# Performance work log

Measured on AMD Instinct MI355X. Metric: run time of the kernel, lower is better.

The kernel has to match this reference:

```python
import jax, jax.numpy as jnp
import numpy as np

N_GENE, N_CELL, D, E = 20000, 50000, 256, 300000

def setup_inputs() -> dict:
    key = jax.random.key(0)
    k1, k2, k3, k4 = jax.random.split(key, 4)
    ufeat = jax.random.normal(k1, (N_GENE, D), dtype=jnp.float32)
    ifeat = jax.random.normal(k2, (N_CELL, D), dtype=jnp.float32)
    src = jax.random.randint(k3, (E,), 0, N_GENE, dtype=jnp.int64 if jax.config.jax_enable_x64 else jnp.int32)
    dst = jax.random.randint(k4, (E,), 0, N_CELL, dtype=jnp.int64 if jax.config.jax_enable_x64 else jnp.int32)
    return {"ufeat": ufeat, "ifeat": ifeat, "src": src, "dst": dst}

def reference(ufeat, ifeat, src, dst):
    # BiDecoder.forward actually executed path: dropout(rate=0.0) == identity,
    # then DGL fn.u_dot_v('h','h','sr') and immediate return of graph.edata['sr'].
    # Per-edge gather + dot product -> shape (E, 1)
    hu = jnp.take(ufeat, src, axis=0)  # (E, D)
    hv = jnp.take(ifeat, dst, axis=0)  # (E, D)
    return jnp.sum(hu * hv, axis=1, keepdims=True)  # (E, 1)
```

## Files before the change

kernel.cpp:

```cpp
#include <hip/hip_runtime.h>
#include <hip/hip_bf16.h>


typedef _Float16 half4 __attribute__((ext_vector_type(4)));
typedef _Float16 half8 __attribute__((ext_vector_type(8)));

__global__ __launch_bounds__(256) void cvt_f32_to_f16(
    const float* __restrict__ u, const float* __restrict__ v,
    _Float16* __restrict__ uh, _Float16* __restrict__ vh,
    int nU, int nTotal)
{
    int i = blockIdx.x * blockDim.x + threadIdx.x;
    const int stride = gridDim.x * blockDim.x;
    const int total8 = nTotal / 8;
    for (; i < total8; i += stride) {
        const int j = i * 8;
        const float* sp;
        _Float16* dp;
        if (j < nU) { sp = u + j;        dp = uh + j; }
        else        { sp = v + (j - nU); dp = vh + (j - nU); }
        const float4 f0 = *reinterpret_cast<const float4*>(sp);
        const float4 f1 = *reinterpret_cast<const float4*>(sp + 4);
        half8 h;
        h[0] = (_Float16)f0.x; h[1] = (_Float16)f0.y;
        h[2] = (_Float16)f0.z; h[3] = (_Float16)f0.w;
        h[4] = (_Float16)f1.x; h[5] = (_Float16)f1.y;
        h[6] = (_Float16)f1.z; h[7] = (_Float16)f1.w;
        *reinterpret_cast<half8*>(dp) = h;
    }
}

__global__ __launch_bounds__(256) void edge_dot_f16(
    const _Float16* __restrict__ uh,
    const _Float16* __restrict__ vh,
    const int* __restrict__ src,
    const int* __restrict__ dst,
    float* __restrict__ out,
    int E)
{
    const int wid  = (blockIdx.x * blockDim.x + threadIdx.x) >> 6;
    const int lane = threadIdx.x & 63;
    const int e0   = wid * 4;
    if (e0 >= E) return;

    const size_t lo = (size_t)lane * 4;

    if (e0 + 3 < E) {
        const int4 sv = *reinterpret_cast<const int4*>(src + e0);
        const int4 tv = *reinterpret_cast<const int4*>(dst + e0);

        const half4 a0 = *reinterpret_cast<const half4*>(uh + (size_t)sv.x * 256 + lo);
        const half4 b0 = *reinterpret_cast<const half4*>(vh + (size_t)tv.x * 256 + lo);
        const half4 a1 = *reinterpret_cast<const half4*>(uh + (size_t)sv.y * 256 + lo);
        const half4 b1 = *reinterpret_cast<const half4*>(vh + (size_t)tv.y * 256 + lo);
        const half4 a2 = *reinterpret_cast<const half4*>(uh + (size_t)sv.z * 256 + lo);
        const half4 b2 = *reinterpret_cast<const half4*>(vh + (size_t)tv.z * 256 + lo);
        const half4 a3 = *reinterpret_cast<const half4*>(uh + (size_t)sv.w * 256 + lo);
        const half4 b3 = *reinterpret_cast<const half4*>(vh + (size_t)tv.w * 256 + lo);

        float u0 = 0.f, u1 = 0.f, u2 = 0.f, u3 = 0.f;
        #pragma unroll
        for (int k = 0; k < 4; ++k) {
            u0 += (float)a0[k] * (float)b0[k];
            u1 += (float)a1[k] * (float)b1[k];
            u2 += (float)a2[k] * (float)b2[k];
            u3 += (float)a3[k] * (float)b3[k];
        }

        #pragma unroll
        for (int off = 32; off > 0; off >>= 1) {
            u0 += __shfl_xor(u0, off, 64);
            u1 += __shfl_xor(u1, off, 64);
            u2 += __shfl_xor(u2, off, 64);
            u3 += __shfl_xor(u3, off, 64);
        }

        float v = u0;
        v = (lane == 1) ? u1 : v;
        v = (lane == 2) ? u2 : v;
        v = (lane == 3) ? u3 : v;
        if (lane < 4) out[e0 + lane] = v;
    } else {
        for (int e = e0; e < E; ++e) {
            const half4 a = *reinterpret_cast<const half4*>(uh + (size_t)src[e] * 256 + lo);
            const half4 b = *reinterpret_cast<const half4*>(vh + (size_t)dst[e] * 256 + lo);
            float u = 0.f;
            #pragma unroll
            for (int k = 0; k < 4; ++k) u += (float)a[k] * (float)b[k];
            #pragma unroll
            for (int off = 32; off > 0; off >>= 1) u += __shfl_xor(u, off, 64);
            if (lane == 0) out[e] = u;
        }
    }
}

__global__ __launch_bounds__(256) void edge_dot_f32(
    const float* __restrict__ ufeat,
    const float* __restrict__ ifeat,
    const int* __restrict__ src,
    const int* __restrict__ dst,
    float* __restrict__ out,
    int E)
{
    const int wid  = (blockIdx.x * blockDim.x + threadIdx.x) >> 6;
    const int lane = threadIdx.x & 63;
    const int e0   = wid * 4;
    if (e0 >= E) return;
    const size_t lo = (size_t)lane * 4;

    for (int e = e0; e < min(e0 + 4, E); ++e) {
        const float4 a = *reinterpret_cast<const float4*>(ufeat + (size_t)src[e] * 256 + lo);
        const float4 b = *reinterpret_cast<const float4*>(ifeat + (size_t)dst[e] * 256 + lo);
        float u = a.x*b.x + a.y*b.y + a.z*b.z + a.w*b.w;
        #pragma unroll
        for (int off = 32; off > 0; off >>= 1) u += __shfl_xor(u, off, 64);
        if (lane == 0) out[e] = u;
    }
}

extern "C" void kernel_launch(void* const* d_in, const int* in_sizes, int n_in,
                              void* d_out, int out_size, void* d_ws, size_t ws_size,
                              hipStream_t stream)
{
    const float* ufeat = (const float*)d_in[0];
    const float* ifeat = (const float*)d_in[1];
    const int*   src   = (const int*)d_in[2];
    const int*   dst   = (const int*)d_in[3];
    float*       out   = (float*)d_out;

    const int E  = in_sizes[2];
    const int nU = in_sizes[0];
    const int nV = in_sizes[1];
    const size_t needBytes = (size_t)(nU + nV) * sizeof(_Float16);

    const int block = 256;
    const int edgesPerBlock = (block / 64) * 4;
    const int grid = (E + edgesPerBlock - 1) / edgesPerBlock;

    if (ws_size >= needBytes) {
        _Float16* uh = (_Float16*)d_ws;
        _Float16* vh = uh + nU;

        const int cvtGrid = 2048;
        cvt_f32_to_f16<<<cvtGrid, block, 0, stream>>>(ufeat, ifeat, uh, vh,
                                                      nU, nU + nV);
        edge_dot_f16<<<grid, block, 0, stream>>>(uh, vh, src, dst, out, E);
    } else {
        edge_dot_f32<<<grid, block, 0, stream>>>(ufeat, ifeat, src, dst, out, E);
    }
}
```

Measured before the change: 60.72 us.

## Bucket edges by destination row range across blocks for L2 locality

The edge-dot kernel now launches 8 blocks per 128-edge chunk. Each block handles only the edges whose destination row falls in its eighth of the cell table, which is meant to make the vh gathers hit a smaller L2/MALL-resident working set. The f32-to-f16 conversion also switches to nontemporal loads. The cost is that every block reads the full dst index array (8x index traffic) and computes per-edge divisions and branches. Each wave also processes edges one at a time with a serialized shuffle reduction, losing the 4-edge ILP of the old kernel.

```diff
diff --git a/kernel.cpp b/kernel.cpp
--- a/kernel.cpp
+++ b/kernel.cpp
@@ -4,6 +4,7 @@
 
 typedef _Float16 half4 __attribute__((ext_vector_type(4)));
 typedef _Float16 half8 __attribute__((ext_vector_type(8)));
+typedef float    f32x4 __attribute__((ext_vector_type(4)));
 
 __global__ __launch_bounds__(256) void cvt_f32_to_f16(
     const float* __restrict__ u, const float* __restrict__ v,
@@ -19,8 +20,8 @@
         _Float16* dp;
         if (j < nU) { sp = u + j;        dp = uh + j; }
         else        { sp = v + (j - nU); dp = vh + (j - nU); }
-        const float4 f0 = *reinterpret_cast<const float4*>(sp);
-        const float4 f1 = *reinterpret_cast<const float4*>(sp + 4);
+        const f32x4 f0 = __builtin_nontemporal_load(reinterpret_cast<const f32x4*>(sp));
+        const f32x4 f1 = __builtin_nontemporal_load(reinterpret_cast<const f32x4*>(sp) + 1);
         half8 h;
         h[0] = (_Float16)f0.x; h[1] = (_Float16)f0.y;
         h[2] = (_Float16)f0.z; h[3] = (_Float16)f0.w;
@@ -30,66 +31,57 @@
     }
 }
 
-__global__ __launch_bounds__(256) void edge_dot_f16(
+__device__ __forceinline__ void dot_one(
+    const _Float16* __restrict__ uh, const _Float16* __restrict__ vh,
+    int s, int t, float* __restrict__ out, int e, int lane, size_t lo)
+{
+    const half4 a = *reinterpret_cast<const half4*>(uh + (size_t)s * 256 + lo);
+    const half4 b = *reinterpret_cast<const half4*>(vh + (size_t)t * 256 + lo);
+    float u = 0.f;
+    #pragma unroll
+    for (int k = 0; k < 4; ++k) u += (float)a[k] * (float)b[k];
+    #pragma unroll
+    for (int off = 32; off > 0; off >>= 1) u += __shfl_xor(u, off, 64);
+    if (lane == 0) out[e] = u;
+}
+
+__global__ __launch_bounds__(256) void edge_dot_f16_bucketed(
     const _Float16* __restrict__ uh,
     const _Float16* __restrict__ vh,
     const int* __restrict__ src,
     const int* __restrict__ dst,
     float* __restrict__ out,
-    int E)
+    int E, unsigned rowsPerBucket)
 {
-    const int wid  = (blockIdx.x * blockDim.x + threadIdx.x) >> 6;
-    const int lane = threadIdx.x & 63;
-    const int e0   = wid * 4;
-    if (e0 >= E) return;
-
+    const unsigned bucket = blockIdx.x & 7;
+    const int chunk = blockIdx.x >> 3;
+    const int wave  = threadIdx.x >> 6;
+    const int lane  = threadIdx.x & 63;
     const size_t lo = (size_t)lane * 4;
 
-    if (e0 + 3 < E) {
-        const int4 sv = *reinterpret_cast<const int4*>(src + e0);
-        const int4 tv = *reinterpret_cast<const int4*>(dst + e0);
+    const int base = chunk * 128 + wave * 32;
+    if (base >= E) return;
+    const int lim = min(base + 32, E);
 
-        const half4 a0 = *reinterpret_cast<const half4*>(uh + (size_t)sv.x * 256 + lo);
-        const half4 b0 = *reinterpret_cast<const half4*>(vh + (size_t)tv.x * 256 + lo);
-        const half4 a1 = *reinterpret_cast<const half4*>(uh + (size_t)sv.y * 256 + lo);
-        const half4 b1 = *reinterpret_cast<const half4*>(vh + (size_t)tv.y * 256 + lo);
-        const half4 a2 = *reinterpret_cast<const half4*>(uh + (size_t)sv.z * 256 + lo);
-        const half4 b2 = *reinterpret_cast<const half4*>(vh + (size_t)tv.z * 256 + lo);
-        const half4 a3 = *reinterpret_cast<const half4*>(uh + (size_t)sv.w * 256 + lo);
-        const half4 b3 = *reinterpret_cast<const half4*>(vh + (size_t)tv.w * 256 + lo);
-
-        float u0 = 0.f, u1 = 0.f, u2 = 0.f, u3 = 0.f;
-        #pragma unroll
-        for (int k = 0; k < 4; ++k) {
-            u0 += (float)a0[k] * (float)b0[k];
-            u1 += (float)a1[k] * (float)b1[k];
-            u2 += (float)a2[k] * (float)b2[k];
-            u3 += (float)a3[k] * (float)b3[k];
-        }
-
-        #pragma unroll
-        for (int off = 32; off > 0; off >>= 1) {
-            u0 += __shfl_xor(u0, off, 64);
-            u1 += __shfl_xor(u1, off, 64);
-            u2 += __shfl_xor(u2, off, 64);
-            u3 += __shfl_xor(u3, off, 64);
-        }
-
-        float v = u0;
-        v = (lane == 1) ? u1 : v;
-        v = (lane == 2) ? u2 : v;
-        v = (lane == 3) ? u3 : v;
-        if (lane < 4) out[e0 + lane] = v;
-    } else {
-        for (int e = e0; e < E; ++e) {
-            const half4 a = *reinterpret_cast<const half4*>(uh + (size_t)src[e] * 256 + lo);
-            const half4 b = *reinterpret_cast<const half4*>(vh + (size_t)dst[e] * 256 + lo);
-            float u = 0.f;
-            #pragma unroll
-            for (int k = 0; k < 4; ++k) u += (float)a[k] * (float)b[k];
-            #pragma unroll
-            for (int off = 32; off > 0; off >>= 1) u += __shfl_xor(u, off, 64);
-            if (lane == 0) out[e] = u;
+    for (int e4 = base; e4 < lim; e4 += 4) {
+        if (e4 + 3 < E) {
+            const int4 tv = *reinterpret_cast<const int4*>(dst + e4);
+            const bool m0 = ((unsigned)tv.x / rowsPerBucket) == bucket;
+            const bool m1 = ((unsigned)tv.y / rowsPerBucket) == bucket;
+            const bool m2 = ((unsigned)tv.z / rowsPerBucket) == bucket;
+            const bool m3 = ((unsigned)tv.w / rowsPerBucket) == bucket;
+            if (!(m0 | m1 | m2 | m3)) continue;
+            const int4 sv = *reinterpret_cast<const int4*>(src + e4);
+            if (m0) dot_one(uh, vh, sv.x, tv.x, out, e4 + 0, lane, lo);
+            if (m1) dot_one(uh, vh, sv.y, tv.y, out, e4 + 1, lane, lo);
+            if (m2) dot_one(uh, vh, sv.z, tv.z, out, e4 + 2, lane, lo);
+            if (m3) dot_one(uh, vh, sv.w, tv.w, out, e4 + 3, lane, lo);
+        } else {
+            for (int e = e4; e < lim; ++e) {
+                const int t = dst[e];
+                if (((unsigned)t / rowsPerBucket) != bucket) continue;
+                dot_one(uh, vh, src[e], t, out, e, lane, lo);
+            }
         }
     }
 }
@@ -128,24 +120,28 @@
     const int*   dst   = (const int*)d_in[3];
     float*       out   = (float*)d_out;
 
-    const int E  = in_sizes[2];
-    const int nU = in_sizes[0];
-    const int nV = in_sizes[1];
+    const int E     = in_sizes[2];
+    const int nU    = in_sizes[0];
+    const int nV    = in_sizes[1];
+    const int nCell = nV / 256;
     const size_t needBytes = (size_t)(nU + nV) * sizeof(_Float16);
 
     const int block = 256;
-    const int edgesPerBlock = (block / 64) * 4;
-    const int grid = (E + edgesPerBlock - 1) / edgesPerBlock;
 
     if (ws_size >= needBytes) {
         _Float16* uh = (_Float16*)d_ws;
         _Float16* vh = uh + nU;
 
-        const int cvtGrid = 2048;
-        cvt_f32_to_f16<<<cvtGrid, block, 0, stream>>>(ufeat, ifeat, uh, vh,
-                                                      nU, nU + nV);
-        edge_dot_f16<<<grid, block, 0, stream>>>(uh, vh, src, dst, out, E);
+        cvt_f32_to_f16<<<2048, block, 0, stream>>>(ufeat, ifeat, uh, vh,
+                                                   nU, nU + nV);
+
+        const unsigned rowsPerBucket = (unsigned)((nCell + 7) / 8);
+        const int nChunks = (E + 127) / 128;
+        edge_dot_f16_bucketed<<<nChunks * 8, block, 0, stream>>>(
+            uh, vh, src, dst, out, E, rowsPerBucket);
     } else {
+        const int edgesPerBlock = (block / 64) * 4;
+        const int grid = (E + edgesPerBlock - 1) / edgesPerBlock;
         edge_dot_f32<<<grid, block, 0, stream>>>(ufeat, ifeat, src, dst, out, E);
     }
 }
```

Measured after the change: 119.0 us. 1.96x slower.
